# Performance work log

Measured on AMD Instinct MI355X. Metric: run time of the kernel, lower is better.

Reference implementation:

```python
import jax, jax.numpy as jnp
import numpy as np

B, C, T = 8, 128, 8192
SIGMA_MIN = 1e-6

def setup_inputs() -> dict:
    key = jax.random.key(0)
    ks = jax.random.split(key, 9)
    x1 = jax.random.normal(ks[0], (B, C, T), dtype=jnp.float32)
    mu = jax.random.normal(ks[1], (B, C, T), dtype=jnp.float32)
    style = jax.random.normal(ks[2], (B, 192), dtype=jnp.float32)
    t_sample = jax.random.uniform(ks[3], (B, 1, 1), dtype=jnp.float32)
    z = jax.random.normal(ks[4], (B, C, T), dtype=jnp.float32)
    W = jax.random.normal(ks[5], (C, C), dtype=jnp.float32) * (1.0 / np.sqrt(C))
    b_lin = jax.random.normal(ks[6], (C,), dtype=jnp.float32) * 0.01
    prompt_lens = jax.random.randint(ks[7], (B,), 64, T // 4)
    x_lens = jax.random.randint(ks[8], (B,), T // 2, T)
    return {"x1": x1, "mu": mu, "style": style, "t_sample": t_sample, "z": z,
            "W": W, "b_lin": b_lin, "x_lens": x_lens, "prompt_lens": prompt_lens}

def reference(x1, mu, style, t_sample, z, W, b_lin, x_lens, prompt_lens):
    # x1, z: [B, C, T]; t_sample: [B, 1, 1]
    sigma = SIGMA_MIN
    Bb, Cc, Tt = x1.shape
    tpos = jnp.arange(Tt)
    pmask = tpos[None, :] < prompt_lens[:, None]            # [B, T] prompt region
    # flow-matching interpolation
    y = (1.0 - (1.0 - sigma) * t_sample) * z + t_sample * x1
    u = x1 - (1.0 - sigma) * z
    # zero out prompt region of y (prompt copy tensor is unused by the mock estimator)
    y = jnp.where(pmask[:, None, :], 0.0, y)
    # mock estimator: per-timestep Linear over channels
    out = jnp.einsum('bct,dc->bdt', y, W) + b_lin[None, :, None]
    # per-sample MSE over [prompt_lens, x_lens) across all channels, then mean over batch
    lmask = (~pmask) & (tpos[None, :] < x_lens[:, None])     # [B, T]
    diff2 = jnp.square(out - u) * lmask[:, None, :]
    counts = (Cc * jnp.sum(lmask, axis=1)).astype(x1.dtype)  # [B]
    loss = jnp.mean(jnp.sum(diff2, axis=(1, 2)) / counts)
    return loss, out + (1.0 - sigma) * z
```

## Files before the change

### kernel.cpp

```cpp
#include <hip/hip_runtime.h>
#include <hip/hip_bf16.h>

#define BB   8
#define CC   128
#define TLEN 8192
#define TBLK 64

typedef __attribute__((ext_vector_type(8))) short short8;
typedef __attribute__((ext_vector_type(4))) float f32x4;

__device__ __forceinline__ short f2bf(float f) {
    union { float f; unsigned u; } v; v.f = f;
    return (short)((v.u + 0x7FFFu + ((v.u >> 16) & 1u)) >> 16);
}
__device__ __forceinline__ float bf2f(unsigned short h) {
    union { unsigned u; float f; } v; v.u = ((unsigned)h) << 16;
    return v.f;
}

__global__ __launch_bounds__(256, 3)
void cfm_main(const float* __restrict__ x1, const float* __restrict__ tsm,
              const float* __restrict__ z, const float* __restrict__ W,
              const float* __restrict__ blin, const int* __restrict__ xlens,
              const int* __restrict__ plens, float* __restrict__ out)
{
    __shared__ short    ylds[TBLK][136];
    __shared__ unsigned uw[TBLK][137];
    __shared__ float    red[256];

    const int b    = blockIdx.y;
    const int t0   = blockIdx.x * TBLK;
    const int tid  = threadIdx.x;
    const int lane = tid & 63;
    const int wid  = tid >> 6;
    const int r15  = lane & 15;
    const int q4   = lane >> 4;

    const float ts  = tsm[b];
    const int   pl  = plens[b];
    const int   xl  = xlens[b];
    const float oms = 0.999999f;
    const float cz  = 1.0f - oms * ts;
    const float cx  = ts;

    short8 afrag[2][4];
    #pragma unroll
    for (int dt = 0; dt < 2; ++dt) {
        const int row = wid * 32 + dt * 16 + r15;
        #pragma unroll
        for (int ks = 0; ks < 4; ++ks) {
            const float4 w0 = *reinterpret_cast<const float4*>(W + row * CC + ks * 32 + q4 * 8);
            const float4 w1 = *reinterpret_cast<const float4*>(W + row * CC + ks * 32 + q4 * 8 + 4);
            short8 a;
            a[0] = f2bf(w0.x); a[1] = f2bf(w0.y); a[2] = f2bf(w0.z); a[3] = f2bf(w0.w);
            a[4] = f2bf(w1.x); a[5] = f2bf(w1.y); a[6] = f2bf(w1.z); a[7] = f2bf(w1.w);
            afrag[dt][ks] = a;
        }
    }

    {
        const int tcol = (tid & 15) * 4;
        const int crow = tid >> 4;
        #pragma unroll
        for (int p = 0; p < 8; ++p) {
            const int c = p * 16 + crow;
            const size_t g = (size_t)(b * CC + c) * TLEN + t0 + tcol;
            const float4 xv = *reinterpret_cast<const float4*>(x1 + g);
            const float4 zv = *reinterpret_cast<const float4*>(z + g);
            const float xa[4] = {xv.x, xv.y, xv.z, xv.w};
            const float za[4] = {zv.x, zv.y, zv.z, zv.w};
            #pragma unroll
            for (int j = 0; j < 4; ++j) {
                const int t = t0 + tcol + j;
                float y = cz * za[j] + cx * xa[j];
                if (t < pl) y = 0.0f;
                ylds[tcol + j][c] = f2bf(y);
                const float w = oms * za[j];
                const float u = xa[j] - w;
                uw[tcol + j][c] = (unsigned)(unsigned short)f2bf(u)
                                | ((unsigned)(unsigned short)f2bf(w) << 16);
            }
        }
    }
    __syncthreads();

    f32x4 acc[2][4];
    #pragma unroll
    for (int dt = 0; dt < 2; ++dt)
        #pragma unroll
        for (int tt = 0; tt < 4; ++tt)
            acc[dt][tt] = (f32x4){0.f, 0.f, 0.f, 0.f};

    #pragma unroll
    for (int ks = 0; ks < 4; ++ks) {
        #pragma unroll
        for (int tt = 0; tt < 4; ++tt) {
            const short8 bfrag =
                *reinterpret_cast<const short8*>(&ylds[tt * 16 + r15][ks * 32 + q4 * 8]);
            acc[0][tt] = __builtin_amdgcn_mfma_f32_16x16x32_bf16(afrag[0][ks], bfrag, acc[0][tt], 0, 0, 0);
            acc[1][tt] = __builtin_amdgcn_mfma_f32_16x16x32_bf16(afrag[1][ks], bfrag, acc[1][tt], 0, 0, 0);
        }
    }

    float bl[2][4];
    #pragma unroll
    for (int dt = 0; dt < 2; ++dt)
        #pragma unroll
        for (int rr = 0; rr < 4; ++rr)
            bl[dt][rr] = blin[wid * 32 + dt * 16 + q4 * 4 + rr];

    float lsum = 0.0f;
    #pragma unroll
    for (int dt = 0; dt < 2; ++dt) {
        #pragma unroll
        for (int tt = 0; tt < 4; ++tt) {
            const int tl = tt * 16 + r15;
            const int t  = t0 + tl;
            const bool lm = (t >= pl) & (t < xl);
            #pragma unroll
            for (int rr = 0; rr < 4; ++rr) {
                const int d = wid * 32 + dt * 16 + q4 * 4 + rr;
                const unsigned uwv = uw[tl][d];
                const float u = bf2f((unsigned short)(uwv & 0xFFFFu));
                const float w = bf2f((unsigned short)(uwv >> 16));
                const float ov = acc[dt][tt][rr] + bl[dt][rr];
                out[1 + (size_t)(b * CC + d) * TLEN + t] = ov + w;
                if (lm) { const float df = ov - u; lsum += df * df; }
            }
        }
    }
    lsum *= 1.0f / (8.0f * 128.0f * (float)(xl - pl));

    red[tid] = lsum;
    __syncthreads();
    for (int s = 128; s >= 1; s >>= 1) {
        if (tid < s) red[tid] += red[tid + s];
        __syncthreads();
    }
    if (tid == 0) atomicAdd(out, red[0]);
}

extern "C" void kernel_launch(void* const* d_in, const int* in_sizes, int n_in,
                              void* d_out, int out_size, void* d_ws, size_t ws_size,
                              hipStream_t stream) {
    const float* x1   = (const float*)d_in[0];
    const float* tsm  = (const float*)d_in[3];
    const float* z    = (const float*)d_in[4];
    const float* W    = (const float*)d_in[5];
    const float* blin = (const float*)d_in[6];
    const int*   xlens = (const int*)d_in[7];
    const int*   plens = (const int*)d_in[8];
    float* out = (float*)d_out;

    hipMemsetAsync(out, 0, sizeof(float), stream);
    dim3 grid(TLEN / TBLK, BB);
    cfm_main<<<grid, 256, 0, stream>>>(x1, tsm, z, W, blin, xlens, plens, out);
}
```

Measured before the change: 35.78 us.

## Halve time tile, pre-pack bf16 W fragments, replace atomics with two-stage reduction

Cuts the time tile from 64 to 32 so twice as many blocks launch, and raises the occupancy hint to 5 blocks per CU. W is converted to bf16 MFMA fragment layout once in a separate prep kernel, so each block loads packed fragments instead of converting fp32 W itself. The per-block tree reduction in shared memory becomes wavefront shuffles, and the global atomicAdd plus memset is replaced by per-block partials summed in a final single-block kernel. This adds two extra kernel launches and gives each block less work over which to spread the fixed W-fragment load.

```diff
diff --git a/kernel.cpp b/kernel.cpp
--- a/kernel.cpp
+++ b/kernel.cpp
@@ -4,7 +4,10 @@
 #define BB   8
 #define CC   128
 #define TLEN 8192
-#define TBLK 64
+#define TBLK 32
+#define NTBLK (TLEN / TBLK)
+#define NBLOCKS (NTBLK * BB)
+#define WS_W_OFF 8192
 
 typedef __attribute__((ext_vector_type(8))) short short8;
 typedef __attribute__((ext_vector_type(4))) float f32x4;
@@ -18,15 +21,30 @@
     return v.f;
 }
 
-__global__ __launch_bounds__(256, 3)
+__global__ void prep_w(const float* __restrict__ W, short* __restrict__ wsW) {
+    const int gid   = blockIdx.x * 256 + threadIdx.x;
+    const int lane  = gid & 63;
+    const int ksdt  = gid >> 6;
+    const int dtile = ksdt >> 2;
+    const int ks    = ksdt & 3;
+    const int row   = dtile * 16 + (lane & 15);
+    const int col0  = ks * 32 + (lane >> 4) * 8;
+    short8 a;
+    #pragma unroll
+    for (int e = 0; e < 8; ++e) a[e] = f2bf(W[row * CC + col0 + e]);
+    reinterpret_cast<short8*>(wsW)[gid] = a;
+}
+
+__global__ __launch_bounds__(256, 5)
 void cfm_main(const float* __restrict__ x1, const float* __restrict__ tsm,
-              const float* __restrict__ z, const float* __restrict__ W,
+              const float* __restrict__ z, const short* __restrict__ wsW,
               const float* __restrict__ blin, const int* __restrict__ xlens,
-              const int* __restrict__ plens, float* __restrict__ out)
+              const int* __restrict__ plens, float* __restrict__ out,
+              float* __restrict__ wsPart)
 {
     __shared__ short    ylds[TBLK][136];
     __shared__ unsigned uw[TBLK][137];
-    __shared__ float    red[256];
+    __shared__ float    red[4];
 
     const int b    = blockIdx.y;
     const int t0   = blockIdx.x * TBLK;
@@ -44,26 +62,21 @@
     const float cx  = ts;
 
     short8 afrag[2][4];
-    #pragma unroll
-    for (int dt = 0; dt < 2; ++dt) {
-        const int row = wid * 32 + dt * 16 + r15;
+    {
+        const short8* wf = reinterpret_cast<const short8*>(wsW);
         #pragma unroll
-        for (int ks = 0; ks < 4; ++ks) {
-            const float4 w0 = *reinterpret_cast<const float4*>(W + row * CC + ks * 32 + q4 * 8);
-            const float4 w1 = *reinterpret_cast<const float4*>(W + row * CC + ks * 32 + q4 * 8 + 4);
-            short8 a;
-            a[0] = f2bf(w0.x); a[1] = f2bf(w0.y); a[2] = f2bf(w0.z); a[3] = f2bf(w0.w);
-            a[4] = f2bf(w1.x); a[5] = f2bf(w1.y); a[6] = f2bf(w1.z); a[7] = f2bf(w1.w);
-            afrag[dt][ks] = a;
-        }
+        for (int dt = 0; dt < 2; ++dt)
+            #pragma unroll
+            for (int ks = 0; ks < 4; ++ks)
+                afrag[dt][ks] = wf[((wid * 2 + dt) * 4 + ks) * 64 + lane];
     }
 
     {
-        const int tcol = (tid & 15) * 4;
-        const int crow = tid >> 4;
+        const int tcol = (tid & 7) * 4;
+        const int crow = tid >> 3;
         #pragma unroll
-        for (int p = 0; p < 8; ++p) {
-            const int c = p * 16 + crow;
+        for (int p = 0; p < 4; ++p) {
+            const int c = p * 32 + crow;
             const size_t g = (size_t)(b * CC + c) * TLEN + t0 + tcol;
             const float4 xv = *reinterpret_cast<const float4*>(x1 + g);
             const float4 zv = *reinterpret_cast<const float4*>(z + g);
@@ -84,17 +97,17 @@
     }
     __syncthreads();
 
-    f32x4 acc[2][4];
+    f32x4 acc[2][2];
     #pragma unroll
     for (int dt = 0; dt < 2; ++dt)
         #pragma unroll
-        for (int tt = 0; tt < 4; ++tt)
+        for (int tt = 0; tt < 2; ++tt)
             acc[dt][tt] = (f32x4){0.f, 0.f, 0.f, 0.f};
 
     #pragma unroll
     for (int ks = 0; ks < 4; ++ks) {
         #pragma unroll
-        for (int tt = 0; tt < 4; ++tt) {
+        for (int tt = 0; tt < 2; ++tt) {
             const short8 bfrag =
                 *reinterpret_cast<const short8*>(&ylds[tt * 16 + r15][ks * 32 + q4 * 8]);
             acc[0][tt] = __builtin_amdgcn_mfma_f32_16x16x32_bf16(afrag[0][ks], bfrag, acc[0][tt], 0, 0, 0);
@@ -113,7 +126,7 @@
     #pragma unroll
     for (int dt = 0; dt < 2; ++dt) {
         #pragma unroll
-        for (int tt = 0; tt < 4; ++tt) {
+        for (int tt = 0; tt < 2; ++tt) {
             const int tl = tt * 16 + r15;
             const int t  = t0 + tl;
             const bool lm = (t >= pl) & (t < xl);
@@ -129,30 +142,48 @@
             }
         }
     }
-    lsum *= 1.0f / (8.0f * 128.0f * (float)(xl - pl));
 
-    red[tid] = lsum;
+    #pragma unroll
+    for (int off = 32; off >= 1; off >>= 1) lsum += __shfl_down(lsum, off);
+    if (lane == 0) red[wid] = lsum;
     __syncthreads();
-    for (int s = 128; s >= 1; s >>= 1) {
-        if (tid < s) red[tid] += red[tid + s];
-        __syncthreads();
+    if (tid == 0) {
+        const float scale = 1.0f / (1024.0f * (float)(xl - pl));
+        wsPart[blockIdx.y * gridDim.x + blockIdx.x] =
+            (red[0] + red[1] + red[2] + red[3]) * scale;
     }
-    if (tid == 0) atomicAdd(out, red[0]);
+}
+
+__global__ void final_red(const float* __restrict__ wsPart, float* __restrict__ out) {
+    __shared__ float red[4];
+    const int tid = threadIdx.x;
+    float s = 0.0f;
+    #pragma unroll
+    for (int i = 0; i < NBLOCKS / 256; ++i) s += wsPart[tid + i * 256];
+    #pragma unroll
+    for (int off = 32; off >= 1; off >>= 1) s += __shfl_down(s, off);
+    if ((tid & 63) == 0) red[tid >> 6] = s;
+    __syncthreads();
+    if (tid == 0) out[0] = red[0] + red[1] + red[2] + red[3];
 }
 
 extern "C" void kernel_launch(void* const* d_in, const int* in_sizes, int n_in,
                               void* d_out, int out_size, void* d_ws, size_t ws_size,
                               hipStream_t stream) {
-    const float* x1   = (const float*)d_in[0];
-    const float* tsm  = (const float*)d_in[3];
-    const float* z    = (const float*)d_in[4];
-    const float* W    = (const float*)d_in[5];
-    const float* blin = (const float*)d_in[6];
+    const float* x1    = (const float*)d_in[0];
+    const float* tsm   = (const float*)d_in[3];
+    const float* z     = (const float*)d_in[4];
+    const float* W     = (const float*)d_in[5];
+    const float* blin  = (const float*)d_in[6];
     const int*   xlens = (const int*)d_in[7];
     const int*   plens = (const int*)d_in[8];
     float* out = (float*)d_out;
 
-    hipMemsetAsync(out, 0, sizeof(float), stream);
-    dim3 grid(TLEN / TBLK, BB);
-    cfm_main<<<grid, 256, 0, stream>>>(x1, tsm, z, W, blin, xlens, plens, out);
+    float* wsPart = (float*)d_ws;
+    short* wsW    = (short*)((char*)d_ws + WS_W_OFF);
+
+    prep_w<<<8, 256, 0, stream>>>(W, wsW);
+    dim3 grid(NTBLK, BB);
+    cfm_main<<<grid, 256, 0, stream>>>(x1, tsm, z, wsW, blin, xlens, plens, out, wsPart);
+    final_red<<<1, 256, 0, stream>>>(wsPart, out);
 }
```

New measurement: 31.59 us. 1.13x faster.
